# Performance work log

Measured on AMD Instinct MI355X. Metric: run time of the kernel, lower is better.

Reference implementation:

```python
import jax, jax.numpy as jnp
import numpy as np
from jax import lax

DT = 0.001   # pytorch_spiking SpikingActivation default dt
EPS = 1e-5   # BatchNorm2d eps
IMG = 64
C = 50       # channel count hard-coded by snn.Convolution(50, 50, ...)


def _conv(x, w):
    # x: NCHW, w: OIHW, valid conv, stride 1 (SpykeTorch snn.Convolution)
    return lax.conv_general_dilated(x, w, (1, 1), 'VALID',
                                    dimension_numbers=('NCHW', 'OIHW', 'NCHW'))


def _sepconv(x, w1, w2, gamma, beta, mean, var):
    # sf.pad(x, (0,2,2,0)): width (left=0,right=2), height (top=2,bottom=0)
    x = jnp.pad(x, ((0, 0), (0, 0), (2, 0), (0, 2)))
    x = _conv(x, w1)                      # k=5 -> H-2, W-2
    inv = lax.rsqrt(var + EPS)            # eval-mode BatchNorm2d with running stats
    x = (x - mean[None, :, None, None]) * (gamma * inv)[None, :, None, None] \
        + beta[None, :, None, None]
    # sf.pad(x, (0,3,3,0)): width (0,3), height (3,0)
    x = jnp.pad(x, ((0, 0), (0, 0), (3, 0), (0, 3)))
    x = _conv(x, w2)                      # k=2 -> back to original H, W
    return x


def _spiking_softmax(x, dt=DT):
    # x: (B, T, J). pytorch_spiking.SpikingActivation(Softmax(-1)):
    # per timestep t: r = softmax(x[:,t]); v += r*dt; s = floor(v); v -= s; out = s/dt
    # straight-through gradient (spiking-aware training): d(out)/dx = d(r)/dx
    xt = jnp.swapaxes(x, 0, 1)            # (T, B, J)

    def step(v, xi):
        r = jax.nn.softmax(xi, axis=-1)
        v = v + r * dt
        s = jnp.floor(v)
        out = r + lax.stop_gradient(s / dt - r)
        return v - s, out

    v0 = jnp.zeros((x.shape[0], x.shape[2]), x.dtype)
    _, ys = lax.scan(step, v0, xt)
    return jnp.swapaxes(ys, 0, 1)         # (B, T, J)


def setup_inputs() -> dict:
    key = jax.random.key(0)
    k0, k1, k2 = jax.random.split(key, 3)
    B = 4
    x = jax.random.normal(k0, (B, IMG * IMG, C), jnp.float32)
    # small-magnitude weights keep the softmax non-degenerate (original init is
    # N(0.8, 0.05), which saturates the softmax; math is identical either way)
    conv1_w = 0.02 * jax.random.normal(k1, (3, C, C, 5, 5), jnp.float32)  # q,k,v
    conv2_w = 0.02 * jax.random.normal(k2, (3, C, C, 2, 2), jnp.float32)
    bn_gamma = jnp.ones((3, C), jnp.float32)
    bn_beta = jnp.zeros((3, C), jnp.float32)
    bn_mean = jnp.zeros((3, C), jnp.float32)
    bn_var = jnp.ones((3, C), jnp.float32)
    return {"x": x, "conv1_w": conv1_w, "conv2_w": conv2_w,
            "bn_gamma": bn_gamma, "bn_beta": bn_beta,
            "bn_mean": bn_mean, "bn_var": bn_var}


def reference(x, conv1_w, conv2_w, bn_gamma, bn_beta, bn_mean, bn_var):
    B = x.shape[0]
    # rearrange 'b (l w) n -> b n l w'
    xi = jnp.transpose(x, (0, 2, 1)).reshape(B, C, IMG, IMG)

    def proj(i):
        t = _sepconv(xi, conv1_w[i], conv2_w[i], bn_gamma[i], bn_beta[i],
                     bn_mean[i], bn_var[i])
        # 'b (h d) l w -> b h (l w) d' with h=1 -> (B, N, d)
        return jnp.swapaxes(t.reshape(B, C, IMG * IMG), 1, 2)

    q, k, v = proj(0), proj(1), proj(2)
    scale = C ** -0.5                      # dim_head ** -0.5
    dots = jnp.einsum('bid,bjd->bij', q, k) * scale   # (B, N, N)
    attn = _spiking_softmax(dots)
    out = jnp.einsum('bij,bjd->bid', attn, v)         # (B, N, d)
    # project_out is False (heads==1 and dim_head==dim) -> identity
    return out
```

## Files before the change

### kernel.cpp

```cpp
#include <hip/hip_runtime.h>
#include <hip/hip_bf16.h>
#include <math.h>

#define NB 4
#define NC 50
#define NN 4096

typedef __attribute__((ext_vector_type(8))) short short8;
typedef __attribute__((ext_vector_type(4))) float f32x4;

static constexpr float F_SCALE = 0.14142135623730951f;
static constexpr float F_LOG2E = 1.44269504088896340f;
static constexpr float F_DT = 0.001f;

static constexpr size_t OFF_XP  = 0;
static constexpr size_t SZ_XP   = (size_t)4*66*68*64/2;
static constexpr size_t OFF_W1T = OFF_XP + SZ_XP;
static constexpr size_t SZ_W1T  = (size_t)3*25*64*64/2;
static constexpr size_t OFF_BI  = OFF_W1T + SZ_W1T;
static constexpr size_t SZ_BI   = 192;
static constexpr size_t OFF_W2T = OFF_BI + SZ_BI;
static constexpr size_t SZ_W2T  = (size_t)3*4*64*64/2;
static constexpr size_t OFF_T1P = OFF_W2T + SZ_W2T;
static constexpr size_t SZ_T1P  = (size_t)12*66*66*64/2;
static constexpr size_t OFF_QB  = OFF_T1P + SZ_T1P;
static constexpr size_t SZ_QB   = (size_t)4*NN*64/2;
static constexpr size_t OFF_KB  = OFF_QB + SZ_QB;
static constexpr size_t SZ_KB   = SZ_QB;
static constexpr size_t OFF_VV  = OFF_KB + SZ_KB;
static constexpr size_t SZ_VV   = (size_t)4*NN*64;
static constexpr size_t OFF_LP  = OFF_VV + SZ_VV;
static constexpr size_t SZ_LP   = (size_t)8*NB*NN;
static constexpr size_t OFF_MP  = OFF_LP + SZ_LP;
static constexpr size_t SZ_MP   = (size_t)8*NB*NN;
static constexpr size_t OFF_GT  = OFF_MP + SZ_MP;
static constexpr size_t OFF_QN2 = OFF_GT + 1;
static constexpr size_t SZ_QN2  = (size_t)NB*NN;
static constexpr size_t OFF_KMX = OFF_QN2 + SZ_QN2;
static constexpr size_t OFF_GN  = OFF_KMX + 1;

__device__ __forceinline__ float bf2f(short s) {
  return __uint_as_float(((unsigned)(unsigned short)s) << 16);
}

__device__ __forceinline__ void stage16(const void* g, void* l) {
  __builtin_amdgcn_global_load_lds(
      (const __attribute__((address_space(1))) unsigned*)g,
      (__attribute__((address_space(3))) unsigned*)l, 16, 0, 0);
}

__global__ __launch_bounds__(256) void k_prep(const float* __restrict__ x,
                                              const float* __restrict__ w1,
                                              const float* __restrict__ w2,
                                              const float* __restrict__ g,
                                              const float* __restrict__ be,
                                              const float* __restrict__ mu,
                                              const float* __restrict__ va,
                                              __hip_bfloat16* __restrict__ xp,
                                              __hip_bfloat16* __restrict__ w1t,
                                              float* __restrict__ bias,
                                              __hip_bfloat16* __restrict__ w2t,
                                              __hip_bfloat16* __restrict__ t1p,
                                              float* __restrict__ out,
                                              float* __restrict__ gateL,
                                              float* __restrict__ gateN,
                                              int* __restrict__ kmx) {
  int bx = blockIdx.x;
  int tid = threadIdx.x;
  if (bx == 0 && tid == 0) {
    gateL[0] = 0.f; gateN[0] = 0.f; kmx[0] = 0;
  }
  if (bx < 4488) {
    int pos = bx * 4 + (tid >> 6);
    int c = tid & 63;
    int b = pos / 4488;
    int rem = pos % 4488;
    int h = rem / 68, w = rem % 68;
    int y = h - 2;
    float v = 0.f;
    if (y >= 0 && y < 64 && w < 64 && c < NC)
      v = x[((size_t)b*NN + y*64 + w)*NC + c];
    xp[(size_t)pos*64 + c] = __float2bfloat16(v);
  } else if (bx < 4575) {
    int bw = bx - 4488;
    if (bw < 75) {
      int p = bw / 25, tap = bw % 25, dy = tap / 5, dx = tap % 5;
      for (int i = tid; i < 4096; i += 256) {
        int oc = i >> 6, c = i & 63;
        float v = 0.f;
        if (oc < NC && c < NC) {
          float sc = g[p*NC+oc] * rsqrtf(va[p*NC+oc] + 1e-5f);
          v = w1[(((size_t)p*NC + oc)*NC + c)*25 + tap] * sc;
        }
        int k = dx*64 + c;
        int ks = dy*10 + (k >> 5), ck = k & 31;
        w1t[(((size_t)p*50 + ks)*64 + oc)*32 + ck] = __float2bfloat16(v);
      }
      if (tap == 0 && tid < 64) {
        int oc = tid;
        float v = 0.f;
        if (oc < NC) {
          float sc = g[p*NC+oc] * rsqrtf(va[p*NC+oc] + 1e-5f);
          v = be[p*NC+oc] - mu[p*NC+oc]*sc;
        }
        bias[p*64 + oc] = v;
      }
    } else {
      int i2 = bw - 75;
      int p = i2 / 4, tap = i2 % 4, dy = tap >> 1, dx = tap & 1;
      for (int i = tid; i < 4096; i += 256) {
        int oc = i >> 6, c = i & 63;
        float v = 0.f;
        if (oc < NC && c < NC)
          v = w2[(((size_t)p*NC + oc)*NC + c)*4 + tap];
        int k = dx*64 + c;
        int ks = dy*4 + (k >> 5), ck = k & 31;
        w2t[(((size_t)p*8 + ks)*64 + oc)*32 + ck] = __float2bfloat16(v);
      }
    }
  } else {
    int bz = bx - 4575;
    if (bz < 1536) {
      int idx = bz * 256 + tid;
      int pb = idx >> 15, r = idx & 32767;
      int h2, w, c;
      if (r < 16896) {
        int hsel = r / 4224;
        h2 = hsel < 3 ? hsel : 65;
        int rem = r % 4224;
        w = rem >> 6; c = rem & 63;
      } else {
        int r2 = r - 16896;
        h2 = 3 + (r2 >> 8);
        int rem = r2 & 255;
        w = 62 + (rem >> 6); c = rem & 63;
      }
      t1p[(((size_t)pb*66 + h2)*66 + w)*64 + c] = __float2bfloat16(0.f);
    } else {
      int i = (bz - 1536) * 256 + tid;
      float4 z = {0.f, 0.f, 0.f, 0.f};
      ((float4*)out)[i] = z;
    }
  }
}

__global__ __launch_bounds__(256, 3) void k_conv1m(const __hip_bfloat16* __restrict__ xp,
                                                   const __hip_bfloat16* __restrict__ w1t,
                                                   const float* __restrict__ bias,
                                                   __hip_bfloat16* __restrict__ t1p) {
  __shared__ char smem[45056 + 8192];
  char* als = smem;
  char* wls = smem + 45056;
  int tid = threadIdx.x;
  int w = tid >> 6, lane = tid & 63;
  int lr = lane & 15, lk = lane >> 4;
  int row = blockIdx.x;
  int pb = blockIdx.y; int p = pb / 4, b = pb % 4;

  const char* awin = (const char*)xp + (((size_t)b*66 + row)*68) * 128;
  const char* wsrc = (const char*)w1t + (size_t)p*50*4096 + w*1024;
  int lanebyte = (lane >> 2)*64 + (((lane & 3) ^ ((lane >> 3) & 3)))*16;
  char* wbuf = wls + w*2048;

#pragma unroll
  for (int it = 0; it < 11; ++it) {
    int L = it*4096 + tid*16;
    int PX = L >> 7;
    int slot = ((L >> 4) ^ PX) & 7;
    stage16(awin + PX*128 + slot*16, als + it*4096 + w*1024);
  }
  stage16(wsrc + lanebyte, wbuf);
  float bv = bias[p*64 + w*16 + lr];
  asm volatile("" :: "v"(bv));
  __syncthreads();

  f32x4 acc0 = {0.f,0.f,0.f,0.f}, acc1 = acc0, acc2 = acc0, acc3 = acc0;
  const char* wrd = wbuf + lr*64 + ((lk ^ ((lr >> 1) & 3)))*16;
  int fb = lr*128 + lk*16;

#pragma unroll
  for (int ks = 0; ks < 50; ++ks) {
    if (ks + 1 < 50) {
      stage16(wsrc + (ks+1)*4096 + lanebyte, wbuf + ((ks+1)&1)*1024);
      asm volatile("s_waitcnt vmcnt(1)" ::: "memory");
    } else {
      asm volatile("s_waitcnt vmcnt(0)" ::: "memory");
    }
    __builtin_amdgcn_sched_barrier(0);
    int dy = ks / 10, kk = ks % 10;
    short8 wv = *(const short8*)(wrd + (ks & 1)*1024);
    int F0 = dy*8704 + kk*64 + fb;
#pragma unroll
    for (int t = 0; t < 4; ++t) {
      int F = F0 + t*2048;
      int lb = (F & ~127) | ((((F >> 4) ^ (F >> 7)) & 7) << 4);
      short8 av = *(const short8*)(als + lb);
      f32x4* ac = (t == 0) ? &acc0 : (t == 1) ? &acc1 : (t == 2) ? &acc2 : &acc3;
      *ac = __builtin_amdgcn_mfma_f32_16x16x32_bf16(av, wv, *ac, 0, 0, 0);
    }
  }

  int h2 = row + 3;
  __hip_bfloat16* orow = t1p + (((size_t)(p*NB + b)*66 + h2)*66)*64;
  f32x4 accs[4] = {acc0, acc1, acc2, acc3};
#pragma unroll
  for (int t = 0; t < 4; ++t) {
#pragma unroll
    for (int r = 0; r < 4; ++r) {
      int j1 = t*16 + lk*4 + r;
      float val = (j1 < 62) ? (accs[t][r] + bv) : 0.f;
      orow[(size_t)j1*64 + w*16 + lr] = __float2bfloat16(val);
    }
  }
}

__global__ __launch_bounds__(256, 3) void k_conv2m(const __hip_bfloat16* __restrict__ t1p,
                                                   const __hip_bfloat16* __restrict__ w2t,
                                                   __hip_bfloat16* __restrict__ qb,
                                                   __hip_bfloat16* __restrict__ kb,
                                                   float* __restrict__ vv,
                                                   float* __restrict__ qn2,
                                                   int* __restrict__ kmx) {
  __shared__ char smem[20480 + 32768];
  char* als = smem;
  char* wls = smem + 20480;
  int tid = threadIdx.x;
  int w = tid >> 6, lane = tid & 63;
  int lr = lane & 15, lk = lane >> 4;
  int row = blockIdx.x;
  int px0 = w * 16;
  int pb = blockIdx.y; int p = pb / 4, b = pb % 4;

  const char* awin = (const char*)t1p + (((size_t)(p*NB + b)*66 + row)*66) * 128;
  const char* wsrc = (const char*)w2t + (size_t)p*8*4096;

#pragma unroll
  for (int it = 0; it < 5; ++it) {
    int L = it*4096 + tid*16;
    int PX = L >> 7;
    int slot = ((L >> 4) ^ PX) & 7;
    stage16(awin + PX*128 + slot*16, als + it*4096 + w*1024);
  }
#pragma unroll
  for (int it = 0; it < 8; ++it)
    stage16(wsrc + it*4096 + tid*16, wls + it*4096 + w*1024);
  __syncthreads();

  f32x4 acc0 = {0.f,0.f,0.f,0.f}, acc1 = acc0, acc2 = acc0, acc3 = acc0;
  int fbase = (px0 + lr)*128 + lk*16;
  const char* wfb = wls + lr*64 + lk*16;

#pragma unroll
  for (int ks = 0; ks < 8; ++ks) {
    int dy = ks >> 2, kk = ks & 3;
    int F = dy*8448 + fbase + kk*64;
    int lb = (F & ~127) | ((((F>>4) ^ (F>>7)) & 7) << 4);
    short8 av = *(const short8*)(als + lb);
    const char* wc = wfb + ks*4096;
    short8 wv0 = *(const short8*)(wc);
    short8 wv1 = *(const short8*)(wc + 1024);
    short8 wv2 = *(const short8*)(wc + 2048);
    short8 wv3 = *(const short8*)(wc + 3072);
    acc0 = __builtin_amdgcn_mfma_f32_16x16x32_bf16(av, wv0, acc0, 0, 0, 0);
    acc1 = __builtin_amdgcn_mfma_f32_16x16x32_bf16(av, wv1, acc1, 0, 0, 0);
    acc2 = __builtin_amdgcn_mfma_f32_16x16x32_bf16(av, wv2, acc2, 0, 0, 0);
    acc3 = __builtin_amdgcn_mfma_f32_16x16x32_bf16(av, wv3, acc3, 0, 0, 0);
  }

  f32x4 accs[4] = {acc0, acc1, acc2, acc3};
  if (p == 0) {
    float sq[4] = {0.f, 0.f, 0.f, 0.f};
#pragma unroll
    for (int nt = 0; nt < 4; ++nt) {
#pragma unroll
      for (int r = 0; r < 4; ++r) {
        int n = row*64 + px0 + lk*4 + r;
        __hip_bfloat16 qv = __float2bfloat16(accs[nt][r] * (F_SCALE * F_LOG2E));
        qb[((size_t)b*NN + n)*64 + nt*16 + lr] = qv;
        float a = bf2f(*(short*)&qv);
        sq[r] += a*a;
      }
    }
#pragma unroll
    for (int r = 0; r < 4; ++r) {
#pragma unroll
      for (int m = 1; m < 16; m <<= 1) sq[r] += __shfl_xor(sq[r], m, 64);
    }
    if (lr == 0) {
#pragma unroll
      for (int r = 0; r < 4; ++r)
        qn2[(size_t)b*NN + row*64 + px0 + lk*4 + r] = sq[r];
    }
  } else if (p == 1) {
    float sk[4] = {0.f, 0.f, 0.f, 0.f};
#pragma unroll
    for (int nt = 0; nt < 4; ++nt) {
#pragma unroll
      for (int r = 0; r < 4; ++r) {
        int n = row*64 + px0 + lk*4 + r;
        __hip_bfloat16 kv = __float2bfloat16(accs[nt][r]);
        kb[((size_t)b*NN + n)*64 + nt*16 + lr] = kv;
        float a = bf2f(*(short*)&kv);
        sk[r] += a*a;
      }
    }
    float mk = fmaxf(fmaxf(sk[0], sk[1]), fmaxf(sk[2], sk[3]));
#pragma unroll
    for (int m = 1; m < 64; m <<= 1) mk = fmaxf(mk, __shfl_xor(mk, m, 64));
    if (lane == 0) atomicMax(kmx, __float_as_int(mk));
  } else {
#pragma unroll
    for (int nt = 0; nt < 4; ++nt) {
#pragma unroll
      for (int r = 0; r < 4; ++r) {
        int n = row*64 + px0 + lk*4 + r;
        vv[((size_t)b*NN + n)*64 + nt*16 + lr] = accs[nt][r];
      }
    }
  }
}

__global__ __launch_bounds__(256) void k_gateB(const float* __restrict__ qn2,
                                               const int* __restrict__ kmx,
                                               float* __restrict__ gateN) {
  int i = blockIdx.x * 256 + threadIdx.x;
  float km = sqrtf(__int_as_float(kmx[0]));
  float term = exp2f(2.f * sqrtf(qn2[i]) * km) * (1.f / (float)NN);
  __shared__ float red[256];
  red[threadIdx.x] = term;
  __syncthreads();
  for (int s = 128; s > 0; s >>= 1) {
    if (threadIdx.x < s) red[threadIdx.x] += red[threadIdx.x + s];
    __syncthreads();
  }
  if (threadIdx.x == 0) atomicAdd(gateN, red[0]);
}

__global__ __launch_bounds__(256) void k_L(const __hip_bfloat16* __restrict__ qb,
                                           const __hip_bfloat16* __restrict__ kb,
                                           const float* __restrict__ gateN,
                                           float* __restrict__ Lpart,
                                           float* __restrict__ Mpart) {
  if (F_DT * gateN[0] < 0.99f) return;
  int w = threadIdx.x >> 6, lane = threadIdx.x & 63;
  int b = blockIdx.z, jc = blockIdx.y;
  int t0 = blockIdx.x * 64 + w * 16;
  int lr = lane & 15, lk = lane >> 4;

  const short* qrow = (const short*)qb + ((size_t)b*NN + t0 + lr)*64 + lk*8;
  short8 a0 = *(const short8*)qrow;
  short8 a1 = *(const short8*)(qrow + 32);
  const short* kp = (const short*)kb + ((size_t)b*NN + jc*512 + lr)*64 + lk*8;

  short8 n00 = *(const short8*)kp;
  short8 n01 = *(const short8*)(kp + 32);
  short8 n10 = *(const short8*)(kp + 1024);
  short8 n11 = *(const short8*)(kp + 1024 + 32);

  float rs[4] = {0.f, 0.f, 0.f, 0.f};
  float mx[4] = {-3e38f, -3e38f, -3e38f, -3e38f};
#pragma unroll 2
  for (int j = 0; j < 512; j += 32) {
    short8 b00 = n00, b01 = n01, b10 = n10, b11 = n11;
    kp += 32*64;
    if (j + 32 < 512) {
      n00 = *(const short8*)kp;
      n01 = *(const short8*)(kp + 32);
      n10 = *(const short8*)(kp + 1024);
      n11 = *(const short8*)(kp + 1024 + 32);
    }
    f32x4 d0 = {0.f,0.f,0.f,0.f}, d1 = {0.f,0.f,0.f,0.f};
    d0 = __builtin_amdgcn_mfma_f32_16x16x32_bf16(a0, b00, d0, 0, 0, 0);
    d0 = __builtin_amdgcn_mfma_f32_16x16x32_bf16(a1, b01, d0, 0, 0, 0);
    d1 = __builtin_amdgcn_mfma_f32_16x16x32_bf16(a0, b10, d1, 0, 0, 0);
    d1 = __builtin_amdgcn_mfma_f32_16x16x32_bf16(a1, b11, d1, 0, 0, 0);
#pragma unroll
    for (int r = 0; r < 4; ++r) {
      rs[r] += exp2f(d0[r]) + exp2f(d1[r]);
      mx[r] = fmaxf(mx[r], fmaxf(d0[r], d1[r]));
    }
  }
#pragma unroll
  for (int r = 0; r < 4; ++r) {
#pragma unroll
    for (int m = 1; m < 16; m <<= 1) {
      rs[r] += __shfl_xor(rs[r], m, 64);
      mx[r] = fmaxf(mx[r], __shfl_xor(mx[r], m, 64));
    }
  }
  if (lr == 0) {
    size_t base = (size_t)jc*(NB*NN) + (size_t)b*NN + t0 + lk*4;
#pragma unroll
    for (int r = 0; r < 4; ++r) {
      Lpart[base + r] = rs[r];
      Mpart[base + r] = mx[r];
    }
  }
}

__global__ __launch_bounds__(256) void k_spike_fb(const __hip_bfloat16* __restrict__ qb,
                                                  const __hip_bfloat16* __restrict__ kb,
                                                  const float* __restrict__ Lpart,
                                                  const float* __restrict__ Mpart,
                                                  const float* __restrict__ gateN,
                                                  const float* __restrict__ vv,
                                                  float* __restrict__ out) {
  if (F_DT * gateN[0] < 0.99f) return;
  int tid = threadIdx.x;
  int b = blockIdx.y;

  __shared__ float Ls[NN];
  __shared__ float red[256];
  float gpart = 0.f;
  for (int t = tid; t < NN; t += 256) {
    float sum = 0.f, mx = -3e38f;
#pragma unroll
    for (int jc = 0; jc < 8; ++jc) {
      sum += Lpart[(size_t)jc*(NB*NN) + (size_t)b*NN + t];
      mx = fmaxf(mx, Mpart[(size_t)jc*(NB*NN) + (size_t)b*NN + t]);
    }
    Ls[t] = sum;
    gpart += exp2f(mx) / sum;
  }
  red[tid] = gpart;
  __syncthreads();
  for (int s = 128; s > 0; s >>= 1) {
    if (tid < s) red[tid] += red[tid + s];
    __syncthreads();
  }
  if (F_DT * red[0] < 0.99f) return;

  int j = blockIdx.x * 256 + tid;
  float kf[64];
  const __hip_bfloat16* kr = kb + ((size_t)b*NN + j)*64;
#pragma unroll
  for (int c = 0; c < 64; ++c) kf[c] = __bfloat162float(kr[c]);
  const __hip_bfloat16* Qb = qb + (size_t)b*NN*64;
  const float* V  = vv + ((size_t)b*NN + j)*64;

  float cum = 0.f, Fprev = 0.f;
  for (int t = 0; t < NN; ++t) {
    const __hip_bfloat16* qr = Qb + (size_t)t*64;
    float dot = 0.f;
    for (int c = 0; c < 64; ++c) dot += __bfloat162float(qr[c]) * kf[c];
    float r = exp2f(dot) / Ls[t];
    cum += r * F_DT;
    float F = floorf(cum);
    if (F > Fprev) {
      float sv = (F - Fprev) / F_DT;
      float* orow = out + ((size_t)b*NN + t)*NC;
      for (int d = 0; d < NC; ++d) atomicAdd(orow + d, sv * V[d]);
      Fprev = F;
    }
  }
}

extern "C" void kernel_launch(void* const* d_in, const int* in_sizes, int n_in,
                              void* d_out, int out_size, void* d_ws, size_t ws_size,
                              hipStream_t stream) {
  const float* x  = (const float*)d_in[0];
  const float* w1 = (const float*)d_in[1];
  const float* w2 = (const float*)d_in[2];
  const float* g  = (const float*)d_in[3];
  const float* be = (const float*)d_in[4];
  const float* mu = (const float*)d_in[5];
  const float* va = (const float*)d_in[6];
  float* out = (float*)d_out;
  float* ws  = (float*)d_ws;

  __hip_bfloat16* xp  = (__hip_bfloat16*)(ws + OFF_XP);
  __hip_bfloat16* w1t = (__hip_bfloat16*)(ws + OFF_W1T);
  float*          bi  = ws + OFF_BI;
  __hip_bfloat16* w2t = (__hip_bfloat16*)(ws + OFF_W2T);
  __hip_bfloat16* t1p = (__hip_bfloat16*)(ws + OFF_T1P);
  __hip_bfloat16* qb  = (__hip_bfloat16*)(ws + OFF_QB);
  __hip_bfloat16* kb  = (__hip_bfloat16*)(ws + OFF_KB);
  float* vv  = ws + OFF_VV;
  float* Lp  = ws + OFF_LP;
  float* Mp  = ws + OFF_MP;
  float* gtL = ws + OFF_GT;
  float* qn2 = ws + OFF_QN2;
  int*   kmx = (int*)(ws + OFF_KMX);
  float* gtN = ws + OFF_GN;

  k_prep  <<<dim3(6911), dim3(256), 0, stream>>>(x, w1, w2, g, be, mu, va,
                                                 xp, w1t, bi, w2t, t1p, out,
                                                 gtL, gtN, kmx);
  k_conv1m<<<dim3(62, 12), dim3(256), 0, stream>>>(xp, w1t, bi, t1p);
  k_conv2m<<<dim3(64, 12), dim3(256), 0, stream>>>(t1p, w2t, qb, kb, vv, qn2, kmx);
  k_gateB <<<dim3(64), dim3(256), 0, stream>>>(qn2, kmx, gtN);
  k_L     <<<dim3(64, 8, NB), dim3(256), 0, stream>>>(qb, kb, gtN, Lp, Mp);
  k_spike_fb<<<dim3(16, NB), dim3(256), 0, stream>>>(qb, kb, Lp, Mp, gtN, vv, out);
}
```

Baseline: 53.09 us.

## Fold gate and row-sum kernels into single gated fallback attention kernel

Removes the separate gate-reduction and MFMA row-sum kernels and merges them into one fallback kernel. Each block recomputes the Cauchy-Schwarz gate over all qn2 values and returns early if the gate shows no spike can fire. This drops two launches and their inter-kernel dependencies from the common path. If the gate passes, the row sums are now computed with scalar loops over the full N×N inside every block, which would be far slower than the old MFMA kernel.

```diff
diff --git a/kernel.cpp b/kernel.cpp
--- a/kernel.cpp
+++ b/kernel.cpp
@@ -29,15 +29,9 @@
 static constexpr size_t SZ_KB   = SZ_QB;
 static constexpr size_t OFF_VV  = OFF_KB + SZ_KB;
 static constexpr size_t SZ_VV   = (size_t)4*NN*64;
-static constexpr size_t OFF_LP  = OFF_VV + SZ_VV;
-static constexpr size_t SZ_LP   = (size_t)8*NB*NN;
-static constexpr size_t OFF_MP  = OFF_LP + SZ_LP;
-static constexpr size_t SZ_MP   = (size_t)8*NB*NN;
-static constexpr size_t OFF_GT  = OFF_MP + SZ_MP;
-static constexpr size_t OFF_QN2 = OFF_GT + 1;
+static constexpr size_t OFF_QN2 = OFF_VV + SZ_VV;
 static constexpr size_t SZ_QN2  = (size_t)NB*NN;
 static constexpr size_t OFF_KMX = OFF_QN2 + SZ_QN2;
-static constexpr size_t OFF_GN  = OFF_KMX + 1;
 
 __device__ __forceinline__ float bf2f(short s) {
   return __uint_as_float(((unsigned)(unsigned short)s) << 16);
@@ -62,14 +56,10 @@
                                               __hip_bfloat16* __restrict__ w2t,
                                               __hip_bfloat16* __restrict__ t1p,
                                               float* __restrict__ out,
-                                              float* __restrict__ gateL,
-                                              float* __restrict__ gateN,
                                               int* __restrict__ kmx) {
   int bx = blockIdx.x;
   int tid = threadIdx.x;
-  if (bx == 0 && tid == 0) {
-    gateL[0] = 0.f; gateN[0] = 0.f; kmx[0] = 0;
-  }
+  if (bx == 0 && tid == 0) kmx[0] = 0;
   if (bx < 4488) {
     int pos = bx * 4 + (tid >> 6);
     int c = tid & 63;
@@ -320,123 +310,56 @@
   }
 }
 
-__global__ __launch_bounds__(256) void k_gateB(const float* __restrict__ qn2,
-                                               const int* __restrict__ kmx,
-                                               float* __restrict__ gateN) {
-  int i = blockIdx.x * 256 + threadIdx.x;
+__global__ __launch_bounds__(256) void k_attn_fb(const __hip_bfloat16* __restrict__ qb,
+                                                 const __hip_bfloat16* __restrict__ kb,
+                                                 const float* __restrict__ qn2,
+                                                 const int* __restrict__ kmx,
+                                                 const float* __restrict__ vv,
+                                                 float* __restrict__ out) {
+  int tid = threadIdx.x;
+  __shared__ float red[256];
+
   float km = sqrtf(__int_as_float(kmx[0]));
-  float term = exp2f(2.f * sqrtf(qn2[i]) * km) * (1.f / (float)NN);
-  __shared__ float red[256];
-  red[threadIdx.x] = term;
-  __syncthreads();
-  for (int s = 128; s > 0; s >>= 1) {
-    if (threadIdx.x < s) red[threadIdx.x] += red[threadIdx.x + s];
-    __syncthreads();
-  }
-  if (threadIdx.x == 0) atomicAdd(gateN, red[0]);
-}
-
-__global__ __launch_bounds__(256) void k_L(const __hip_bfloat16* __restrict__ qb,
-                                           const __hip_bfloat16* __restrict__ kb,
-                                           const float* __restrict__ gateN,
-                                           float* __restrict__ Lpart,
-                                           float* __restrict__ Mpart) {
-  if (F_DT * gateN[0] < 0.99f) return;
-  int w = threadIdx.x >> 6, lane = threadIdx.x & 63;
-  int b = blockIdx.z, jc = blockIdx.y;
-  int t0 = blockIdx.x * 64 + w * 16;
-  int lr = lane & 15, lk = lane >> 4;
-
-  const short* qrow = (const short*)qb + ((size_t)b*NN + t0 + lr)*64 + lk*8;
-  short8 a0 = *(const short8*)qrow;
-  short8 a1 = *(const short8*)(qrow + 32);
-  const short* kp = (const short*)kb + ((size_t)b*NN + jc*512 + lr)*64 + lk*8;
-
-  short8 n00 = *(const short8*)kp;
-  short8 n01 = *(const short8*)(kp + 32);
-  short8 n10 = *(const short8*)(kp + 1024);
-  short8 n11 = *(const short8*)(kp + 1024 + 32);
-
-  float rs[4] = {0.f, 0.f, 0.f, 0.f};
-  float mx[4] = {-3e38f, -3e38f, -3e38f, -3e38f};
-#pragma unroll 2
-  for (int j = 0; j < 512; j += 32) {
-    short8 b00 = n00, b01 = n01, b10 = n10, b11 = n11;
-    kp += 32*64;
-    if (j + 32 < 512) {
-      n00 = *(const short8*)kp;
-      n01 = *(const short8*)(kp + 32);
-      n10 = *(const short8*)(kp + 1024);
-      n11 = *(const short8*)(kp + 1024 + 32);
-    }
-    f32x4 d0 = {0.f,0.f,0.f,0.f}, d1 = {0.f,0.f,0.f,0.f};
-    d0 = __builtin_amdgcn_mfma_f32_16x16x32_bf16(a0, b00, d0, 0, 0, 0);
-    d0 = __builtin_amdgcn_mfma_f32_16x16x32_bf16(a1, b01, d0, 0, 0, 0);
-    d1 = __builtin_amdgcn_mfma_f32_16x16x32_bf16(a0, b10, d1, 0, 0, 0);
-    d1 = __builtin_amdgcn_mfma_f32_16x16x32_bf16(a1, b11, d1, 0, 0, 0);
-#pragma unroll
-    for (int r = 0; r < 4; ++r) {
-      rs[r] += exp2f(d0[r]) + exp2f(d1[r]);
-      mx[r] = fmaxf(mx[r], fmaxf(d0[r], d1[r]));
-    }
-  }
-#pragma unroll
-  for (int r = 0; r < 4; ++r) {
-#pragma unroll
-    for (int m = 1; m < 16; m <<= 1) {
-      rs[r] += __shfl_xor(rs[r], m, 64);
-      mx[r] = fmaxf(mx[r], __shfl_xor(mx[r], m, 64));
-    }
-  }
-  if (lr == 0) {
-    size_t base = (size_t)jc*(NB*NN) + (size_t)b*NN + t0 + lk*4;
-#pragma unroll
-    for (int r = 0; r < 4; ++r) {
-      Lpart[base + r] = rs[r];
-      Mpart[base + r] = mx[r];
-    }
-  }
-}
-
-__global__ __launch_bounds__(256) void k_spike_fb(const __hip_bfloat16* __restrict__ qb,
-                                                  const __hip_bfloat16* __restrict__ kb,
-                                                  const float* __restrict__ Lpart,
-                                                  const float* __restrict__ Mpart,
-                                                  const float* __restrict__ gateN,
-                                                  const float* __restrict__ vv,
-                                                  float* __restrict__ out) {
-  if (F_DT * gateN[0] < 0.99f) return;
-  int tid = threadIdx.x;
-  int b = blockIdx.y;
-
-  __shared__ float Ls[NN];
-  __shared__ float red[256];
-  float gpart = 0.f;
-  for (int t = tid; t < NN; t += 256) {
-    float sum = 0.f, mx = -3e38f;
-#pragma unroll
-    for (int jc = 0; jc < 8; ++jc) {
-      sum += Lpart[(size_t)jc*(NB*NN) + (size_t)b*NN + t];
-      mx = fmaxf(mx, Mpart[(size_t)jc*(NB*NN) + (size_t)b*NN + t]);
-    }
-    Ls[t] = sum;
-    gpart += exp2f(mx) / sum;
-  }
-  red[tid] = gpart;
+  float part = 0.f;
+  const float4* q4 = (const float4*)qn2;
+  for (int i = tid; i < NB*NN/4; i += 256) {
+    float4 v = q4[i];
+    part += exp2f(2.f*sqrtf(v.x)*km) + exp2f(2.f*sqrtf(v.y)*km)
+          + exp2f(2.f*sqrtf(v.z)*km) + exp2f(2.f*sqrtf(v.w)*km);
+  }
+  red[tid] = part;
   __syncthreads();
   for (int s = 128; s > 0; s >>= 1) {
     if (tid < s) red[tid] += red[tid + s];
     __syncthreads();
   }
-  if (F_DT * red[0] < 0.99f) return;
+  float gate = red[0] * (1.f / (float)NN);
+  if (F_DT * gate < 0.99f) return;
+
+  int b = blockIdx.y;
+  __shared__ float Ls[NN];
+  const __hip_bfloat16* Qb = qb + (size_t)b*NN*64;
+  const __hip_bfloat16* Kb = kb + (size_t)b*NN*64;
+  for (int t = tid; t < NN; t += 256) {
+    float qf[64];
+    const __hip_bfloat16* qr = Qb + (size_t)t*64;
+    for (int c = 0; c < 64; ++c) qf[c] = __bfloat162float(qr[c]);
+    float s = 0.f;
+    for (int j = 0; j < NN; ++j) {
+      const __hip_bfloat16* krow = Kb + (size_t)j*64;
+      float dot = 0.f;
+      for (int c = 0; c < 64; ++c) dot += qf[c] * __bfloat162float(krow[c]);
+      s += exp2f(dot);
+    }
+    Ls[t] = s;
+  }
+  __syncthreads();
 
   int j = blockIdx.x * 256 + tid;
   float kf[64];
-  const __hip_bfloat16* kr = kb + ((size_t)b*NN + j)*64;
-#pragma unroll
+  const __hip_bfloat16* kr = Kb + (size_t)j*64;
   for (int c = 0; c < 64; ++c) kf[c] = __bfloat162float(kr[c]);
-  const __hip_bfloat16* Qb = qb + (size_t)b*NN*64;
-  const float* V  = vv + ((size_t)b*NN + j)*64;
+  const float* V = vv + ((size_t)b*NN + j)*64;
 
   float cum = 0.f, Fprev = 0.f;
   for (int t = 0; t < NN; ++t) {
@@ -476,19 +399,12 @@
   __hip_bfloat16* qb  = (__hip_bfloat16*)(ws + OFF_QB);
   __hip_bfloat16* kb  = (__hip_bfloat16*)(ws + OFF_KB);
   float* vv  = ws + OFF_VV;
-  float* Lp  = ws + OFF_LP;
-  float* Mp  = ws + OFF_MP;
-  float* gtL = ws + OFF_GT;
   float* qn2 = ws + OFF_QN2;
   int*   kmx = (int*)(ws + OFF_KMX);
-  float* gtN = ws + OFF_GN;
-
-  k_prep  <<<dim3(6911), dim3(256), 0, stream>>>(x, w1, w2, g, be, mu, va,
-                                                 xp, w1t, bi, w2t, t1p, out,
-                                                 gtL, gtN, kmx);
-  k_conv1m<<<dim3(62, 12), dim3(256), 0, stream>>>(xp, w1t, bi, t1p);
-  k_conv2m<<<dim3(64, 12), dim3(256), 0, stream>>>(t1p, w2t, qb, kb, vv, qn2, kmx);
-  k_gateB <<<dim3(64), dim3(256), 0, stream>>>(qn2, kmx, gtN);
-  k_L     <<<dim3(64, 8, NB), dim3(256), 0, stream>>>(qb, kb, gtN, Lp, Mp);
-  k_spike_fb<<<dim3(16, NB), dim3(256), 0, stream>>>(qb, kb, Lp, Mp, gtN, vv, out);
-}
+
+  k_prep   <<<dim3(6911), dim3(256), 0, stream>>>(x, w1, w2, g, be, mu, va,
+                                                  xp, w1t, bi, w2t, t1p, out, kmx);
+  k_conv1m <<<dim3(62, 12), dim3(256), 0, stream>>>(xp, w1t, bi, t1p);
+  k_conv2m <<<dim3(64, 12), dim3(256), 0, stream>>>(t1p, w2t, qb, kb, vv, qn2, kmx);
+  k_attn_fb<<<dim3(16, NB), dim3(256), 0, stream>>>(qb, kb, qn2, kmx, vv, out);
+}
```

Result: slower. 55.88 us (+5.3%).
